# Performance work log

Hardware: AMD Instinct MI355X
Metric: run time of the kernel (lower is better)

The kernel has to match this reference:

```python
import jax, jax.numpy as jnp
import numpy as np

EPS_DIST = 1e-10
BN_EPS = 1e-5
K = 3  # nsample / three_nn


def setup_inputs() -> dict:
    key = jax.random.key(0)
    ks = jax.random.split(key, 8)
    B, N, S, D1, D2 = 4, 8192, 2048, 128, 256
    C_in = D1 + D2  # 384
    H = 256
    inp = {
        "pos1": jax.random.normal(ks[0], (B, 3, N), dtype=jnp.float32),
        "pos2": jax.random.normal(ks[1], (B, 3, S), dtype=jnp.float32),
        "feature1": jax.random.normal(ks[2], (B, D1, N), dtype=jnp.float32),
        "feature2": jax.random.normal(ks[3], (B, D2, S), dtype=jnp.float32),
        # MLP layer 1: Conv1d(384->256, k=1) + BN
        "W1": jax.random.normal(ks[4], (H, C_in), dtype=jnp.float32) * (1.0 / np.sqrt(C_in)),
        "b1": jnp.zeros((H,), dtype=jnp.float32),
        "g1": jnp.ones((H,), dtype=jnp.float32),
        "be1": jnp.zeros((H,), dtype=jnp.float32),
        # MLP layer 2: Conv1d(256->256, k=1) + BN
        "W2": jax.random.normal(ks[5], (H, H), dtype=jnp.float32) * (1.0 / np.sqrt(H)),
        "b2": jnp.zeros((H,), dtype=jnp.float32),
        "g2": jnp.ones((H,), dtype=jnp.float32),
        "be2": jnp.zeros((H,), dtype=jnp.float32),
    }
    return inp


def _conv_bn_relu(x, W, b, gamma, beta):
    # x: [B, Cin, N]; 1x1 Conv1d == channel GEMM
    y = jnp.einsum("oc,bcn->bon", W, x) + b[None, :, None]
    # BatchNorm1d in training mode: batch statistics over (B, N)
    mean = jnp.mean(y, axis=(0, 2), keepdims=True)
    var = jnp.mean(jnp.square(y - mean), axis=(0, 2), keepdims=True)
    y = (y - mean) * jax.lax.rsqrt(var + BN_EPS)
    y = y * gamma[None, :, None] + beta[None, :, None]
    return jax.nn.relu(y)


def reference(pos1, pos2, feature1, feature2, W1, b1, g1, be1, W2, b2, g2, be2):
    # pos1: [B,3,N], pos2: [B,3,S], feature1: [B,D1,N], feature2: [B,D2,S]
    p1 = jnp.swapaxes(pos1, 1, 2)  # [B,N,3]
    p2 = jnp.swapaxes(pos2, 1, 2)  # [B,S,3]
    # three_nn: squared-distance 3-NN of each point in p1 among p2
    d2 = (jnp.sum(p1 * p1, -1)[:, :, None]
          + jnp.sum(p2 * p2, -1)[:, None, :]
          - 2.0 * jnp.einsum("bnc,bsc->bns", p1, p2))  # [B,N,S]
    neg_vals, idx = jax.lax.top_k(-d2, K)  # idx: [B,N,3]
    dists = jnp.maximum(-neg_vals, EPS_DIST)  # dists[dists<1e-10]=1e-10
    w = 1.0 / dists
    w = w / jnp.sum(w, -1, keepdims=True)  # [B,N,3]
    # grouping_operation: gather feature2 [B,D,S] by idx -> [B,D,N,3]
    grouped = jax.vmap(lambda f, i: f[:, i])(feature2, idx)
    interpolated = jnp.sum(grouped * w[:, None, :, :], axis=-1)  # [B,D2,N]
    feat = jnp.concatenate([interpolated, feature1], axis=1)  # [B,384,N]
    feat = _conv_bn_relu(feat, W1, b1, g1, be1)
    feat = _conv_bn_relu(feat, W2, b2, g2, be2)
    return feat  # [B,256,N]
```

## Files before the change

kernel.cpp:

```cpp
#include <hip/hip_runtime.h>
#include <hip/hip_bf16.h>
#include <cstdint>

typedef unsigned short u16;
typedef unsigned int u32;
typedef unsigned long long u64;
typedef __bf16 bf16x8 __attribute__((ext_vector_type(8)));
typedef float f32x4 __attribute__((ext_vector_type(4)));
typedef u16 u16x8 __attribute__((ext_vector_type(8)));

__device__ __forceinline__ u16 f2b(float f) {
    unsigned int u = __float_as_uint(f);
    u += 0x7fffu + ((u >> 16) & 1u);
    return (u16)(u >> 16);
}
__device__ __forceinline__ float b2f(u16 h) {
    return __uint_as_float(((unsigned int)h) << 16);
}
__device__ __forceinline__ void async_cp16(void* lds, const void* g) {
    __builtin_amdgcn_global_load_lds((const __attribute__((address_space(1))) void*)g,
                                     (__attribute__((address_space(3))) void*)lds, 16, 0, 0);
}
__device__ __forceinline__ u32 fmono(float f) {
    u32 u = __float_as_uint(f);
    return u ^ (((u32)((int)u >> 31)) | 0x80000000u);
}
__device__ __forceinline__ u64 shfl_xor_u64(u64 v, int mask) {
    u32 lo = (u32)v, hi = (u32)(v >> 32);
    lo = (u32)__shfl_xor((int)lo, mask);
    hi = (u32)__shfl_xor((int)hi, mask);
    return ((u64)hi << 32) | lo;
}
__device__ __forceinline__ void ins3(u64 k, u64& k0, u64& k1, u64& k2) {
    bool c0 = k > k0, c1 = k > k1, c2 = k > k2;
    k2 = c1 ? k1 : (c2 ? k : k2);
    k1 = c0 ? k0 : (c1 ? k : k1);
    k0 = c0 ? k : k0;
}
__device__ __forceinline__ int pkix(int i) { return i + (i >> 6); }

#define NB_NN  1024
#define NB_CVT 160
#define NB_T2  512
#define NB_T1  1024

__global__ __launch_bounds__(256, 8) void prep_kernel(const float* __restrict__ w1,
                                                      const float* __restrict__ w2,
                                                      u16* __restrict__ wb,
                                                      const float* __restrict__ feature2,
                                                      u16* __restrict__ f2t,
                                                      const float* __restrict__ feature1,
                                                      u16* __restrict__ f1t,
                                                      const float* __restrict__ pos1,
                                                      const float* __restrict__ pos2,
                                                      int* __restrict__ idx_out,
                                                      float* __restrict__ w_out) {
    __shared__ __align__(16) char smem[19712];
    int bi = blockIdx.x;
    int tid = threadIdx.x;

    if (bi >= NB_NN) {
        int ci = bi - NB_NN;
        if (ci < NB_CVT) {
            int i = ci * 256 + tid;
            if (i < 40960) {
                const float* src = (i < 24576) ? w1 : w2;
                int k = (i < 24576) ? i : (i - 24576);
                float4 v = *(const float4*)&src[(size_t)k * 4];
                ushort4 o;
                o.x = f2b(v.x); o.y = f2b(v.y); o.z = f2b(v.z); o.w = f2b(v.w);
                *(ushort4*)&wb[(size_t)i * 4] = o;
            }
            return;
        }
        float (*t)[65] = (float (*)[65])smem;
        const float* in; u16* out; int C, S, s0, c0, b;
        if (ci < NB_CVT + NB_T2) {
            int lin = ci - NB_CVT;
            C = 256; S = 2048; in = feature2; out = f2t;
            s0 = (lin & 31) * 64; c0 = ((lin >> 5) & 3) * 64; b = lin >> 7;
        } else {
            int lin = ci - NB_CVT - NB_T2;
            C = 128; S = 8192; in = feature1; out = f1t;
            s0 = (lin & 127) * 64; c0 = ((lin >> 7) & 1) * 64; b = lin >> 8;
        }
        const float* ib = in + (size_t)b * C * S;
        u16* ob = out + (size_t)b * S * C;
        int col = tid & 63, r0 = tid >> 6;
#pragma unroll
        for (int p = 0; p < 16; ++p) {
            int c = p * 4 + r0;
            t[c][col] = ib[(size_t)(c0 + c) * S + s0 + col];
        }
        __syncthreads();
#pragma unroll
        for (int p = 0; p < 16; ++p) {
            int s = p * 4 + r0;
            ob[(size_t)(s0 + s) * C + c0 + col] = f2b(t[col][s]);
        }
        return;
    }

    float4* pk = (float4*)smem;
    u64* warr = (u64*)(smem + 16640);
    int j0 = bi * 32;
    int b = j0 >> 13;
    const float* p2 = pos2 + (size_t)b * 3 * 2048;
    int p = tid & 15, ck = tid >> 4;
    int wv = tid >> 6, lane = tid & 63;
    int na = (j0 & 8191) + p, nbq = na + 16;
    const float* p1 = pos1 + (size_t)b * 3 * 8192;
    float xa = p1[na], ya = p1[8192 + na], za = p1[16384 + na];
    float xb = p1[nbq], yb = p1[8192 + nbq], zb = p1[16384 + nbq];

    u64 a0k = 0, a1k = 0, a2k = 0, b0k = 0, b1k = 0, b2k = 0;

    for (int half = 0; half < 2; ++half) {
        int hbase = half * 1024;
        for (int i = tid; i < 1024; i += 256) {
            int s = hbase + i;
            float x = p2[s], y = p2[2048 + s], z = p2[4096 + s];
            pk[pkix(i)] = make_float4(x, y, z, -0.5f * (x * x + y * y + z * z));
        }
        __syncthreads();

        float ga0 = -3.4e38f, ga1 = -3.4e38f, ga2 = -3.4e38f;
        float gb0 = -3.4e38f, gb1 = -3.4e38f, gb2 = -3.4e38f;
        int ia0 = 0, ia1 = 0, ia2 = 0, ib0 = 0, ib1 = 0, ib2 = 0;
        int sb = ck * 64;
        const float4* pc = pk + pkix(sb);
#pragma unroll 4
        for (int it = 0; it < 64; ++it) {
            float4 cd = pc[it];
            int s = sb + it;
            float ta = fmaf(xa, cd.x, fmaf(ya, cd.y, fmaf(za, cd.z, cd.w)));
            float tb = fmaf(xb, cd.x, fmaf(yb, cd.y, fmaf(zb, cd.z, cd.w)));
            bool a0 = ta > ga0, a1 = ta > ga1, a2 = ta > ga2;
            ga2 = a1 ? ga1 : (a2 ? ta : ga2);
            ia2 = a1 ? ia1 : (a2 ? s : ia2);
            ga1 = a0 ? ga0 : (a1 ? ta : ga1);
            ia1 = a0 ? ia0 : (a1 ? s : ia1);
            ga0 = a0 ? ta : ga0;
            ia0 = a0 ? s : ia0;
            bool b0c = tb > gb0, b1c = tb > gb1, b2c = tb > gb2;
            gb2 = b1c ? gb1 : (b2c ? tb : gb2);
            ib2 = b1c ? ib1 : (b2c ? s : ib2);
            gb1 = b0c ? gb0 : (b1c ? tb : gb1);
            ib1 = b0c ? ib0 : (b1c ? s : ib1);
            gb0 = b0c ? tb : gb0;
            ib0 = b0c ? s : ib0;
        }
        __syncthreads();

        int gi0 = hbase + ia0, gi1 = hbase + ia1, gi2 = hbase + ia2;
        int gj0 = hbase + ib0, gj1 = hbase + ib1, gj2 = hbase + ib2;
        ins3(((u64)fmono(ga0) << 32) | (u64)(2047 - gi0), a0k, a1k, a2k);
        ins3(((u64)fmono(ga1) << 32) | (u64)(2047 - gi1), a0k, a1k, a2k);
        ins3(((u64)fmono(ga2) << 32) | (u64)(2047 - gi2), a0k, a1k, a2k);
        ins3(((u64)fmono(gb0) << 32) | (u64)(2047 - gj0), b0k, b1k, b2k);
        ins3(((u64)fmono(gb1) << 32) | (u64)(2047 - gj1), b0k, b1k, b2k);
        ins3(((u64)fmono(gb2) << 32) | (u64)(2047 - gj2), b0k, b1k, b2k);
    }

#pragma unroll
    for (int mask = 16; mask <= 32; mask <<= 1) {
        u64 pa0 = shfl_xor_u64(a0k, mask), pa1 = shfl_xor_u64(a1k, mask), pa2 = shfl_xor_u64(a2k, mask);
        u64 pb0 = shfl_xor_u64(b0k, mask), pb1 = shfl_xor_u64(b1k, mask), pb2 = shfl_xor_u64(b2k, mask);
        ins3(pa0, a0k, a1k, a2k); ins3(pa1, a0k, a1k, a2k); ins3(pa2, a0k, a1k, a2k);
        ins3(pb0, b0k, b1k, b2k); ins3(pb1, b0k, b1k, b2k); ins3(pb2, b0k, b1k, b2k);
    }
    if (lane < 16) {
        u64* wr = &warr[(wv * 16 + p) * 6];
        wr[0] = a0k; wr[1] = a1k; wr[2] = a2k;
        wr[3] = b0k; wr[4] = b1k; wr[5] = b2k;
    }
    __syncthreads();
    if (tid < 32) {
        int q = tid;
        int pp = q & 15, off = (q < 16) ? 0 : 3;
        const u64* w0 = &warr[pp * 6];
        u64 k0 = w0[off], k1 = w0[off + 1], k2 = w0[off + 2];
#pragma unroll
        for (int w = 1; w < 4; ++w) {
            const u64* wr = &warr[(w * 16 + pp) * 6];
            ins3(wr[off], k0, k1, k2);
            ins3(wr[off + 1], k0, k1, k2);
            ins3(wr[off + 2], k0, k1, k2);
        }
        int s0 = 2047 - (int)(k0 & 0xFFFFFFFFu);
        int s1 = 2047 - (int)(k1 & 0xFFFFFFFFu);
        int s2 = 2047 - (int)(k2 & 0xFFFFFFFFu);
        int j = j0 + q;
        int n = j & 8191;
        float x1 = p1[n], y1 = p1[8192 + n], z1 = p1[16384 + n];
        float n1 = x1 * x1 + y1 * y1 + z1 * z1;
        float X0 = p2[s0], Y0 = p2[2048 + s0], Z0 = p2[4096 + s0];
        float X1 = p2[s1], Y1v = p2[2048 + s1], Z1 = p2[4096 + s1];
        float X2 = p2[s2], Y2v = p2[2048 + s2], Z2 = p2[4096 + s2];
        float t0 = x1 * X0 + y1 * Y0 + z1 * Z0 - 0.5f * (X0 * X0 + Y0 * Y0 + Z0 * Z0);
        float t1 = x1 * X1 + y1 * Y1v + z1 * Z1 - 0.5f * (X1 * X1 + Y1v * Y1v + Z1 * Z1);
        float t2 = x1 * X2 + y1 * Y2v + z1 * Z2 - 0.5f * (X2 * X2 + Y2v * Y2v + Z2 * Z2);
        float d0 = fmaxf(fmaf(-2.f, t0, n1), 1e-10f);
        float d1 = fmaxf(fmaf(-2.f, t1, n1), 1e-10f);
        float d2 = fmaxf(fmaf(-2.f, t2, n1), 1e-10f);
        float w0v = 1.f / d0, w1v = 1.f / d1, w2v = 1.f / d2;
        float inv = 1.f / (w0v + w1v + w2v);
        idx_out[j * 3] = s0; idx_out[j * 3 + 1] = s1; idx_out[j * 3 + 2] = s2;
        w_out[j * 3] = w0v * inv; w_out[j * 3 + 1] = w1v * inv; w_out[j * 3 + 2] = w2v * inv;
    }
}

__global__ __launch_bounds__(256) void gather_kernel(const u16* __restrict__ f2t,
                                                     const int* __restrict__ idx,
                                                     const float* __restrict__ wgt,
                                                     u16* __restrict__ interp) {
    int wv = threadIdx.x >> 6, lane = threadIdx.x & 63;
    int j = blockIdx.x * 4 + wv;
    int b = j >> 13;
    int i0 = idx[j * 3], i1 = idx[j * 3 + 1], i2 = idx[j * 3 + 2];
    float w0 = wgt[j * 3], w1 = wgt[j * 3 + 1], w2 = wgt[j * 3 + 2];
    const u16* r0 = f2t + ((size_t)(b * 2048 + i0)) * 256;
    const u16* r1 = f2t + ((size_t)(b * 2048 + i1)) * 256;
    const u16* r2 = f2t + ((size_t)(b * 2048 + i2)) * 256;
    int c = lane * 4;
    ushort4 v0 = *(const ushort4*)(r0 + c);
    ushort4 v1 = *(const ushort4*)(r1 + c);
    ushort4 v2 = *(const ushort4*)(r2 + c);
    ushort4 o;
    o.x = f2b(w0 * b2f(v0.x) + w1 * b2f(v1.x) + w2 * b2f(v2.x));
    o.y = f2b(w0 * b2f(v0.y) + w1 * b2f(v1.y) + w2 * b2f(v2.y));
    o.z = f2b(w0 * b2f(v0.z) + w1 * b2f(v1.z) + w2 * b2f(v2.z));
    o.w = f2b(w0 * b2f(v0.w) + w1 * b2f(v1.w) + w2 * b2f(v2.w));
    *(ushort4*)(interp + (size_t)j * 256 + c) = o;
}

template <int KT, bool SPLIT, bool FUSE>
__global__ __launch_bounds__(256, 2) void gemm_kernel(const u16* __restrict__ A1,
                                                      const u16* __restrict__ A2,
                                                      const u16* __restrict__ Bw,
                                                      const float* __restrict__ bias,
                                                      const float* __restrict__ stats_in,
                                                      const float* __restrict__ g_in,
                                                      const float* __restrict__ be_in,
                                                      u16* __restrict__ Yb,
                                                      float* __restrict__ stats) {
    __shared__ u16 Al[128 * 64];
    __shared__ u16 Bl[128 * 64];
    int tid = threadIdx.x;
    int lane = tid & 63, wv = tid >> 6;
    int j0 = blockIdx.x * 128, m0 = blockIdx.y * 128;
    int l15 = lane & 15, q = lane >> 4;
    int wj = (wv >> 1) * 64, wm = (wv & 1) * 64;
    f32x4 acc[4][4];
#pragma unroll
    for (int i = 0; i < 4; ++i)
#pragma unroll
        for (int jj = 0; jj < 4; ++jj) acc[i][jj] = (f32x4){0.f, 0.f, 0.f, 0.f};

    int rbase = wv * 32;
    int lrow = lane >> 3, lchunk = lane & 7;
    const u16* Bg = Bw + (size_t)m0 * KT;

    for (int k0 = 0; k0 < KT; k0 += 64) {
        if (FUSE) {
            int c = k0 + lchunk * 8;
            const float inv = 1.f / 32768.f;
            float aa[8], ssv[8];
#pragma unroll
            for (int e = 0; e < 8; e += 4) {
                float4 sm = *(const float4*)&stats_in[c + e];
                float4 sq = *(const float4*)&stats_in[256 + c + e];
                float4 gg = *(const float4*)&g_in[c + e];
                float4 bb = *(const float4*)&be_in[c + e];
                float m, v;
                m = sm.x * inv; v = sq.x * inv - m * m; aa[e + 0] = gg.x * rsqrtf(v + 1e-5f); ssv[e + 0] = bb.x - m * aa[e + 0];
                m = sm.y * inv; v = sq.y * inv - m * m; aa[e + 1] = gg.y * rsqrtf(v + 1e-5f); ssv[e + 1] = bb.y - m * aa[e + 1];
                m = sm.z * inv; v = sq.z * inv - m * m; aa[e + 2] = gg.z * rsqrtf(v + 1e-5f); ssv[e + 2] = bb.z - m * aa[e + 2];
                m = sm.w * inv; v = sq.w * inv - m * m; aa[e + 3] = gg.w * rsqrtf(v + 1e-5f); ssv[e + 3] = bb.w - m * aa[e + 3];
            }
#pragma unroll
            for (int qq = 0; qq < 4; ++qq) {
                int row = rbase + qq * 8;
                u16x8 y = *(const u16x8*)&A1[(size_t)(j0 + row + lrow) * 256 + c];
                u16x8 o;
#pragma unroll
                for (int e = 0; e < 8; ++e)
                    o[e] = f2b(fmaxf(b2f(y[e]) * aa[e] + ssv[e], 0.f));
                *(u16x8*)&Al[(row + lrow) * 64 + lchunk * 8] = o;
                async_cp16(&Bl[row * 64], Bg + (size_t)(row + lrow) * KT + k0 + lchunk * 8);
            }
        } else {
            const u16* src; int stride;
            if (!SPLIT || k0 < 256) { src = A1 + (size_t)j0 * 256 + k0; stride = 256; }
            else                    { src = A2 + (size_t)j0 * 128 + (k0 - 256); stride = 128; }
#pragma unroll
            for (int qq = 0; qq < 4; ++qq) {
                int row = rbase + qq * 8;
                async_cp16(&Al[row * 64], src + (size_t)(row + lrow) * stride + lchunk * 8);
                async_cp16(&Bl[row * 64], Bg + (size_t)(row + lrow) * KT + k0 + lchunk * 8);
            }
        }
        __syncthreads();
#pragma unroll
        for (int ks = 0; ks < 2; ++ks) {
            bf16x8 af[4], bfr[4];
#pragma unroll
            for (int i = 0; i < 4; ++i)
                af[i] = *(const bf16x8*)&Al[(wj + i * 16 + l15) * 64 + ks * 32 + q * 8];
#pragma unroll
            for (int i = 0; i < 4; ++i)
                bfr[i] = *(const bf16x8*)&Bl[(wm + i * 16 + l15) * 64 + ks * 32 + q * 8];
#pragma unroll
            for (int i = 0; i < 4; ++i)
#pragma unroll
                for (int jj = 0; jj < 4; ++jj)
                    acc[i][jj] = __builtin_amdgcn_mfma_f32_16x16x32_bf16(af[i], bfr[jj],
                                                                         acc[i][jj], 0, 0, 0);
        }
        __syncthreads();
    }
#pragma unroll
    for (int jj = 0; jj < 4; ++jj) {
        int m = m0 + wm + jj * 16 + l15;
        float bv = bias[m];
        float s = 0.f, s2 = 0.f;
#pragma unroll
        for (int i = 0; i < 4; ++i) {
            int jr = j0 + wj + i * 16 + q * 4;
#pragma unroll
            for (int r = 0; r < 4; ++r) {
                float v = acc[i][jj][r] + bv;
                s += v; s2 += v * v;
                Yb[(size_t)(jr + r) * 256 + m] = f2b(v);
            }
        }
        s += __shfl_xor(s, 16); s += __shfl_xor(s, 32);
        s2 += __shfl_xor(s2, 16); s2 += __shfl_xor(s2, 32);
        if (q == 0) {
            atomicAdd(&stats[m], s);
            atomicAdd(&stats[256 + m], s2);
        }
    }
}

__global__ __launch_bounds__(256) void final_out_kernel(const u16* __restrict__ Y2,
                                                        const float* __restrict__ stats,
                                                        const float* __restrict__ g,
                                                        const float* __restrict__ be,
                                                        float* __restrict__ out) {
    __shared__ float t[64][65];
    int j0 = blockIdx.x * 64, o0 = blockIdx.y * 64;
    int tid = threadIdx.x;
    int c4 = (tid & 15) * 4, rw = tid >> 4;
#pragma unroll
    for (int p = 0; p < 4; ++p) {
        int jl = p * 16 + rw;
        ushort4 v = *(const ushort4*)&Y2[(size_t)(j0 + jl) * 256 + o0 + c4];
        t[jl][c4] = b2f(v.x); t[jl][c4 + 1] = b2f(v.y);
        t[jl][c4 + 2] = b2f(v.z); t[jl][c4 + 3] = b2f(v.w);
    }
    __syncthreads();
    int b = j0 >> 13, n0 = j0 & 8191;
    const float inv = 1.f / 32768.f;
#pragma unroll
    for (int p = 0; p < 4; ++p) {
        int ol = p * 16 + rw;
        int o = o0 + ol;
        float mean = stats[o] * inv;
        float var = stats[256 + o] * inv - mean * mean;
        float a = g[o] * rsqrtf(var + 1e-5f);
        float s = be[o] - mean * a;
        float4 v;
        v.x = fmaxf(t[c4][ol] * a + s, 0.f);
        v.y = fmaxf(t[c4 + 1][ol] * a + s, 0.f);
        v.z = fmaxf(t[c4 + 2][ol] * a + s, 0.f);
        v.w = fmaxf(t[c4 + 3][ol] * a + s, 0.f);
        *(float4*)&out[(size_t)b * 2097152 + (size_t)o * 8192 + n0 + c4] = v;
    }
}

extern "C" void kernel_launch(void* const* d_in, const int* in_sizes, int n_in,
                              void* d_out, int out_size, void* d_ws, size_t ws_size,
                              hipStream_t stream) {
    const float* pos1 = (const float*)d_in[0];
    const float* pos2 = (const float*)d_in[1];
    const float* feature1 = (const float*)d_in[2];
    const float* feature2 = (const float*)d_in[3];
    const float* W1 = (const float*)d_in[4];
    const float* b1 = (const float*)d_in[5];
    const float* g1 = (const float*)d_in[6];
    const float* be1 = (const float*)d_in[7];
    const float* W2 = (const float*)d_in[8];
    const float* b2 = (const float*)d_in[9];
    const float* g2 = (const float*)d_in[10];
    const float* be2 = (const float*)d_in[11];

    char* ws = (char*)d_ws;
    int*   IDX    = (int*)(ws + 0);
    float* WGT    = (float*)(ws + 393216);
    u16*   W1B    = (u16*)(ws + 786432);
    u16*   W2B    = (u16*)(ws + 983040);
    float* STATS  = (float*)(ws + 1114112);
    u16*   F2T    = (u16*)(ws + 1118208);
    u16*   F1T    = (u16*)(ws + 5312512);
    u16*   INTERP = (u16*)(ws + 13701120);
    u16*   Y1     = (u16*)(ws + 30478336);
    u16*   Y2     = (u16*)(ws + 47255552);
    float* OUT    = (float*)d_out;

    hipMemsetAsync(STATS, 0, 1024 * sizeof(float), stream);
    prep_kernel<<<NB_NN + NB_CVT + NB_T2 + NB_T1, 256, 0, stream>>>(
        W1, W2, W1B, feature2, F2T, feature1, F1T, pos1, pos2, IDX, WGT);
    gather_kernel<<<8192, 256, 0, stream>>>(F2T, IDX, WGT, INTERP);
    gemm_kernel<384, true, false><<<dim3(256, 2), 256, 0, stream>>>(
        INTERP, F1T, W1B, b1, nullptr, nullptr, nullptr, Y1, STATS);
    gemm_kernel<256, false, true><<<dim3(256, 2), 256, 0, stream>>>(
        Y1, nullptr, W2B, b2, STATS, g1, be1, Y2, STATS + 512);
    final_out_kernel<<<dim3(512, 4), 256, 0, stream>>>(Y2, STATS + 512, g2, be2, OUT);
}
```

Before: 204.6 us.

## Stage GEMM epilogue through LDS for coalesced stores; precompute BN table once

The GEMM epilogue now writes bf16 results into a padded LDS tile, then issues 16-byte coalesced row stores to global memory instead of scattered 2-byte stores. Separately, the fused BN+ReLU path computes per-channel scale/shift once per block into an LDS table rather than recomputing rsqrt from global stats every k-step. Shared memory grows to about 36KB per block, which may affect occupancy at two blocks per CU, and adds a barrier before the store phase.

```diff
diff --git a/kernel.cpp b/kernel.cpp
--- a/kernel.cpp
+++ b/kernel.cpp
@@ -244,8 +244,11 @@
                                                       const float* __restrict__ be_in,
                                                       u16* __restrict__ Yb,
                                                       float* __restrict__ stats) {
-    __shared__ u16 Al[128 * 64];
-    __shared__ u16 Bl[128 * 64];
+    __shared__ __align__(16) char smemA[36864];
+    u16* Al = (u16*)smemA;
+    u16* Bl = (u16*)(smemA + 16384);
+    u16* T  = (u16*)smemA;
+    float2* BNT = (float2*)(smemA + 34816);
     int tid = threadIdx.x;
     int lane = tid & 63, wv = tid >> 6;
     int j0 = blockIdx.x * 128, m0 = blockIdx.y * 128;
@@ -257,6 +260,16 @@
 #pragma unroll
         for (int jj = 0; jj < 4; ++jj) acc[i][jj] = (f32x4){0.f, 0.f, 0.f, 0.f};
 
+    if (FUSE) {
+        int m = tid;
+        const float inv = 1.f / 32768.f;
+        float mean = stats_in[m] * inv;
+        float var = stats_in[256 + m] * inv - mean * mean;
+        float a = g_in[m] * rsqrtf(var + 1e-5f);
+        BNT[m] = make_float2(a, be_in[m] - mean * a);
+        __syncthreads();
+    }
+
     int rbase = wv * 32;
     int lrow = lane >> 3, lchunk = lane & 7;
     const u16* Bg = Bw + (size_t)m0 * KT;
@@ -264,20 +277,9 @@
     for (int k0 = 0; k0 < KT; k0 += 64) {
         if (FUSE) {
             int c = k0 + lchunk * 8;
-            const float inv = 1.f / 32768.f;
-            float aa[8], ssv[8];
-#pragma unroll
-            for (int e = 0; e < 8; e += 4) {
-                float4 sm = *(const float4*)&stats_in[c + e];
-                float4 sq = *(const float4*)&stats_in[256 + c + e];
-                float4 gg = *(const float4*)&g_in[c + e];
-                float4 bb = *(const float4*)&be_in[c + e];
-                float m, v;
-                m = sm.x * inv; v = sq.x * inv - m * m; aa[e + 0] = gg.x * rsqrtf(v + 1e-5f); ssv[e + 0] = bb.x - m * aa[e + 0];
-                m = sm.y * inv; v = sq.y * inv - m * m; aa[e + 1] = gg.y * rsqrtf(v + 1e-5f); ssv[e + 1] = bb.y - m * aa[e + 1];
-                m = sm.z * inv; v = sq.z * inv - m * m; aa[e + 2] = gg.z * rsqrtf(v + 1e-5f); ssv[e + 2] = bb.z - m * aa[e + 2];
-                m = sm.w * inv; v = sq.w * inv - m * m; aa[e + 3] = gg.w * rsqrtf(v + 1e-5f); ssv[e + 3] = bb.w - m * aa[e + 3];
-            }
+            float2 bn[8];
+#pragma unroll
+            for (int e = 0; e < 8; ++e) bn[e] = BNT[c + e];
 #pragma unroll
             for (int qq = 0; qq < 4; ++qq) {
                 int row = rbase + qq * 8;
@@ -285,7 +287,7 @@
                 u16x8 o;
 #pragma unroll
                 for (int e = 0; e < 8; ++e)
-                    o[e] = f2b(fmaxf(b2f(y[e]) * aa[e] + ssv[e], 0.f));
+                    o[e] = f2b(fmaxf(b2f(y[e]) * bn[e].x + bn[e].y, 0.f));
                 *(u16x8*)&Al[(row + lrow) * 64 + lchunk * 8] = o;
                 async_cp16(&Bl[row * 64], Bg + (size_t)(row + lrow) * KT + k0 + lchunk * 8);
             }
@@ -321,25 +323,32 @@
     }
 #pragma unroll
     for (int jj = 0; jj < 4; ++jj) {
-        int m = m0 + wm + jj * 16 + l15;
-        float bv = bias[m];
+        int ml = wm + jj * 16 + l15;
+        float bv = bias[m0 + ml];
         float s = 0.f, s2 = 0.f;
 #pragma unroll
         for (int i = 0; i < 4; ++i) {
-            int jr = j0 + wj + i * 16 + q * 4;
+            int jl = wj + i * 16 + q * 4;
 #pragma unroll
             for (int r = 0; r < 4; ++r) {
                 float v = acc[i][jj][r] + bv;
                 s += v; s2 += v * v;
-                Yb[(size_t)(jr + r) * 256 + m] = f2b(v);
+                T[(jl + r) * 136 + ml] = f2b(v);
             }
         }
         s += __shfl_xor(s, 16); s += __shfl_xor(s, 32);
         s2 += __shfl_xor(s2, 16); s2 += __shfl_xor(s2, 32);
         if (q == 0) {
-            atomicAdd(&stats[m], s);
-            atomicAdd(&stats[256 + m], s2);
-        }
+            atomicAdd(&stats[m0 + ml], s);
+            atomicAdd(&stats[256 + m0 + ml], s2);
+        }
+    }
+    __syncthreads();
+#pragma unroll
+    for (int it = 0; it < 8; ++it) {
+        int jl = it * 16 + wv * 4 + q;
+        u16x8 v = *(const u16x8*)&T[jl * 136 + l15 * 8];
+        *(u16x8*)&Yb[(size_t)(j0 + jl) * 256 + m0 + l15 * 8] = v;
     }
 }
 
```

New measurement: 201.9 us. About the same (-1.4%).
